# Performance work log

Measured on AMD Instinct MI355X. Metric: run time of the kernel, lower is better.

Reference implementation:

```python
import jax, jax.numpy as jnp
import numpy as np

T, B, I = 1024, 32, 1024   # seq_len, batch, input_size
H = 1024                   # hidden_size
NH = 8                     # n_heads
HS = H // NH               # head_size = 128


def setup_inputs() -> dict:
    key = jax.random.key(0)
    kx, kih, khh, kb = jax.random.split(key, 4)
    lim = (1.0 / HS) ** 0.5
    xs = jax.random.normal(kx, (T, B, I), dtype=jnp.float32)
    weight_ih = jax.random.uniform(kih, (NH, 4 * HS, I), minval=-lim, maxval=lim, dtype=jnp.float32)
    weight_hh = jax.random.uniform(khh, (NH, 4 * HS, HS), minval=-lim, maxval=lim, dtype=jnp.float32)
    bias = jax.random.uniform(kb, (NH, 4 * HS), minval=-lim, maxval=lim, dtype=jnp.float32)
    return {"xs": xs, "weight_ih": weight_ih, "weight_hh": weight_hh, "bias": bias}


def reference(xs, weight_ih, weight_hh, bias):
    # xs: [T, B, I]; weight_ih: [NH, 4*HS, I]; weight_hh: [NH, 4*HS, HS]; bias: [NH, 4*HS]
    t, b, _ = xs.shape
    nh, k4, hs = weight_hh.shape
    zeros = jnp.zeros((b, nh, hs), dtype=xs.dtype)

    def step(state, x):
        h, c, m, n = state  # each [B, NH, HS]
        lin = (jnp.einsum('hki,bi->bhk', weight_ih, x)
               + jnp.einsum('hkd,bhd->bhk', weight_hh, h)
               + bias)  # [B, NH, 4*HS]
        i, f, z, o = jnp.split(lin, 4, axis=2)
        z = jnp.tanh(z)
        o = jax.nn.sigmoid(o)
        m_new = jnp.maximum(f + m, i)          # stabilizer state
        i_e = jnp.exp(i - m_new)
        f_e = jnp.exp(f + m - m_new)
        c_new = f_e * c + i_e * z
        n_new = f_e * n + i_e
        h_new = o * (c_new / n_new)
        return (h_new, c_new, m_new, n_new), h_new.reshape(b, nh * hs)

    _, hs_out = jax.lax.scan(step, (zeros, zeros, zeros, zeros), xs)
    return hs_out  # [T, B, H]
```

## Files before the change

### kernel.cpp

```cpp
#include <hip/hip_runtime.h>
#include <stdint.h>
#include <stddef.h>

#define TT   1024
#define BB   32
#define II   1024
#define HH   1024
#define NHH  8
#define HSS  128
#define N4   4096

typedef _Float16 h8 __attribute__((ext_vector_type(8)));
typedef _Float16 h4 __attribute__((ext_vector_type(4)));
typedef float    f4 __attribute__((ext_vector_type(4)));

#define GLDS16(G, L) __builtin_amdgcn_global_load_lds(                      \
    (__attribute__((address_space(1))) void*)(G),                           \
    (__attribute__((address_space(3))) void*)(L), 16, 0, 0)

__global__ void prep_kernel(const float* __restrict__ whh, float* __restrict__ whhT,
                            float* __restrict__ st, float* __restrict__ hst) {
  int idx = blockIdx.x * blockDim.x + threadIdx.x;
  int stride = gridDim.x * blockDim.x;
  for (int i = idx; i < NHH * 512 * HSS; i += stride) {
    int head = i >> 16;
    int rem = i & 65535;
    int n = rem >> 7, k = rem & 127;
    whhT[(size_t)(head * HSS + k) * 512 + n] = whh[i];
  }
  for (int i = idx; i < 3 * BB * NHH * HSS; i += stride) st[i] = 0.0f;
  for (int i = idx; i < BB * NHH * HSS; i += stride) hst[i] = 0.0f;
}

__global__ __launch_bounds__(256) void convert_split(
    const float* __restrict__ src, _Float16* __restrict__ hi,
    _Float16* __restrict__ lo, int n4) {
  int idx = blockIdx.x * blockDim.x + threadIdx.x;
  int stride = gridDim.x * blockDim.x;
  for (int i = idx; i < n4; i += stride) {
    const float4 x = *(const float4*)&src[(size_t)i * 4];
    _Float16 h0 = (_Float16)x.x, h1 = (_Float16)x.y,
             h2 = (_Float16)x.z, h3 = (_Float16)x.w;
    _Float16 l0 = (_Float16)((x.x - (float)h0) * 2048.0f);
    _Float16 l1 = (_Float16)((x.y - (float)h1) * 2048.0f);
    _Float16 l2 = (_Float16)((x.z - (float)h2) * 2048.0f);
    _Float16 l3 = (_Float16)((x.w - (float)h3) * 2048.0f);
    h4 hv = {h0, h1, h2, h3};
    h4 lv = {l0, l1, l2, l3};
    *(h4*)&hi[(size_t)i * 4] = hv;
    *(h4*)&lo[(size_t)i * 4] = lv;
  }
}

__global__ __launch_bounds__(256, 2) void gemm_gates_mfma(
    const _Float16* __restrict__ Ah, const _Float16* __restrict__ Al,
    const _Float16* __restrict__ Bh, const _Float16* __restrict__ Bl,
    const float* __restrict__ bias, float* __restrict__ C) {
  __shared__ __align__(16) _Float16 sAh[128 * 32];
  __shared__ __align__(16) _Float16 sAl[128 * 32];
  __shared__ __align__(16) _Float16 sBh[128 * 32];
  __shared__ __align__(16) _Float16 sBl[128 * 32];

  const int tid = threadIdx.x;
  const int lane = tid & 63;
  const int wave = tid >> 6;
  const long r0 = (long)blockIdx.y * 128;
  const long c0 = (long)blockIdx.x * 128;
  const int wr = (wave >> 1) * 64;
  const int wc = (wave & 1) * 64;

  f4 acc1[4][4], acc2[4][4];
#pragma unroll
  for (int i = 0; i < 4; ++i)
#pragma unroll
    for (int j = 0; j < 4; ++j) { acc1[i][j] = (f4)0.0f; acc2[i][j] = (f4)0.0f; }

  const int sRow = tid >> 2;
  const int sKh = (tid & 3) * 8;
  const _Float16* gAh = Ah + (r0 + sRow) * 1024 + sKh;
  const _Float16* gAl = Al + (r0 + sRow) * 1024 + sKh;
  const _Float16* gBh = Bh + (c0 + sRow) * 1024 + sKh;
  const _Float16* gBl = Bl + (c0 + sRow) * 1024 + sKh;
  _Float16* lAh = &sAh[sRow * 32 + sKh];
  _Float16* lAl = &sAl[sRow * 32 + sKh];
  _Float16* lBh = &sBh[sRow * 32 + sKh];
  _Float16* lBl = &sBl[sRow * 32 + sKh];

  const int fRow = lane & 15;
  const int fK = (lane >> 4) * 8;

  for (int kt = 0; kt < 32; ++kt) {
    const int k0 = kt * 32;
    GLDS16(gAh + k0, lAh);
    GLDS16(gAh + k0 + 64 * 1024, lAh + 64 * 32);
    GLDS16(gAl + k0, lAl);
    GLDS16(gAl + k0 + 64 * 1024, lAl + 64 * 32);
    GLDS16(gBh + k0, lBh);
    GLDS16(gBh + k0 + 64 * 1024, lBh + 64 * 32);
    GLDS16(gBl + k0, lBl);
    GLDS16(gBl + k0 + 64 * 1024, lBl + 64 * 32);
    __syncthreads();

    h8 fBh[4], fBl[4];
#pragma unroll
    for (int j = 0; j < 4; ++j) {
      fBh[j] = *(const h8*)&sBh[(wc + j * 16 + fRow) * 32 + fK];
      fBl[j] = *(const h8*)&sBl[(wc + j * 16 + fRow) * 32 + fK];
    }
#pragma unroll
    for (int i = 0; i < 4; ++i) {
      h8 ah = *(const h8*)&sAh[(wr + i * 16 + fRow) * 32 + fK];
      h8 al = *(const h8*)&sAl[(wr + i * 16 + fRow) * 32 + fK];
#pragma unroll
      for (int j = 0; j < 4; ++j) {
        acc1[i][j] = __builtin_amdgcn_mfma_f32_16x16x32_f16(ah, fBh[j], acc1[i][j], 0, 0, 0);
        acc2[i][j] = __builtin_amdgcn_mfma_f32_16x16x32_f16(ah, fBl[j], acc2[i][j], 0, 0, 0);
        acc2[i][j] = __builtin_amdgcn_mfma_f32_16x16x32_f16(al, fBh[j], acc2[i][j], 0, 0, 0);
      }
    }
    __syncthreads();
  }

  const int rgrp = (lane >> 4) * 4;
#pragma unroll
  for (int j = 0; j < 4; ++j) {
    const long col = c0 + wc + j * 16 + fRow;
    const float bj = bias[col];
#pragma unroll
    for (int i = 0; i < 4; ++i) {
      const long row = r0 + wr + i * 16 + rgrp;
#pragma unroll
      for (int q = 0; q < 4; ++q) {
        C[(row + q) * (long)N4 + col] =
            acc1[i][j][q] + acc2[i][j][q] * (1.0f / 2048.0f) + bj;
      }
    }
  }
}

__device__ __forceinline__ float fast_sigmoid(float x) {
  return 1.0f / (1.0f + __expf(-x));
}
__device__ __forceinline__ float fast_tanh(float x) {
  return 1.0f - 2.0f / (__expf(2.0f * x) + 1.0f);
}

__global__ __launch_bounds__(512, 2) void scan_f32(
    const float* __restrict__ gates, const float* __restrict__ whhT,
    float* __restrict__ out,
    float* __restrict__ stc, float* __restrict__ stn, float* __restrict__ stm,
    float* __restrict__ hst, int t0, int chp) {
  __shared__ float hbuf[128];
  __shared__ float pre[512];
  const int tid = threadIdx.x;
  const int head = blockIdx.x >> 5, b = blockIdx.x & 31;
  const int g = tid >> 7;

  float W[128];
#pragma unroll
  for (int k = 0; k < 128; ++k) W[k] = whhT[(size_t)(head * HSS + k) * 512 + tid];

  float c = 0.f, nn = 0.f, m = 0.f;
  if (tid < 128) {
    int si = (b * NHH + head) * HSS + tid;
    c = stc[si]; nn = stn[si]; m = stm[si];
    hbuf[tid] = hst[si];
  }
  __syncthreads();

  const size_t gbase = (size_t)b * N4 + head * 512 + tid;
  float gcur = gates[gbase];

  for (int t = 0; t < chp; ++t) {
    float gnext = 0.0f;
    if (t + 1 < chp) gnext = gates[gbase + (size_t)(t + 1) * 32 * N4];

    float a0 = 0.f, a1 = 0.f;
#pragma unroll
    for (int k4 = 0; k4 < 16; ++k4) {
      float4 h0 = *(const float4*)&hbuf[k4 * 4];
      float4 h1 = *(const float4*)&hbuf[64 + k4 * 4];
      a0 = fmaf(W[k4 * 4 + 0], h0.x, a0); a0 = fmaf(W[k4 * 4 + 1], h0.y, a0);
      a0 = fmaf(W[k4 * 4 + 2], h0.z, a0); a0 = fmaf(W[k4 * 4 + 3], h0.w, a0);
      a1 = fmaf(W[64 + k4 * 4 + 0], h1.x, a1); a1 = fmaf(W[64 + k4 * 4 + 1], h1.y, a1);
      a1 = fmaf(W[64 + k4 * 4 + 2], h1.z, a1); a1 = fmaf(W[64 + k4 * 4 + 3], h1.w, a1);
    }
    float pv = gcur + (a0 + a1);
    if (g == 2) pv = fast_tanh(pv);
    else if (g == 3) pv = fast_sigmoid(pv);
    pre[tid] = pv;
    __syncthreads();

    if (tid < 128) {
      float iv = pre[tid], fv = pre[128 + tid];
      float zt = pre[256 + tid], og = pre[384 + tid];
      float a = fv + m;
      float mn = fmaxf(a, iv);
      float fe = __expf(a - mn);
      float ie = __expf(iv - mn);
      c = fe * c + ie * zt;
      nn = fe * nn + ie;
      m = mn;
      float h = og * (c / nn);
      out[(size_t)(t0 + t) * (BB * HH) + (size_t)b * HH + head * HSS + tid] = h;
      hbuf[tid] = h;
    }
    __syncthreads();
    gcur = gnext;
  }

  if (tid < 128) {
    int si = (b * NHH + head) * HSS + tid;
    stc[si] = c; stn[si] = nn; stm[si] = m;
    hst[si] = hbuf[tid];
  }
}

extern "C" void kernel_launch(void* const* d_in, const int* in_sizes, int n_in,
                              void* d_out, int out_size, void* d_ws, size_t ws_size,
                              hipStream_t stream) {
  const float* xs   = (const float*)d_in[0];
  const float* wih  = (const float*)d_in[1];
  const float* whh  = (const float*)d_in[2];
  const float* bias = (const float*)d_in[3];
  float* out = (float*)d_out;
  char* ws = (char*)d_ws;

  float* whhT = (float*)(ws + 0);
  float* stc  = (float*)(ws + 2097152);
  float* stn  = (float*)(ws + 2228224);
  float* stm  = (float*)(ws + 2359296);
  float* hst  = (float*)(ws + 2490368);
  _Float16* Bh = (_Float16*)(ws + 2621440);
  _Float16* Bl = (_Float16*)(ws + 11010048);
  const size_t base = 19398656;

  int ch = 256;
  while (ch > 8 && base + (size_t)ch * 655360 > ws_size) ch >>= 1;
  _Float16* Ahp = (_Float16*)(ws + base);
  _Float16* Alp = (_Float16*)(ws + base + (size_t)ch * 65536);
  float* gts = (float*)(ws + base + (size_t)ch * 131072);
  const int nch = TT / ch;

  prep_kernel<<<256, 256, 0, stream>>>(whh, whhT, stc, hst);
  convert_split<<<1024, 256, 0, stream>>>(wih, Bh, Bl, N4 * II / 4);

  for (int cix = 0; cix < nch; ++cix) {
    convert_split<<<1024, 256, 0, stream>>>(xs + (size_t)cix * ch * BB * II,
                                            Ahp, Alp, ch * BB * II / 4);
    dim3 g(32, (unsigned)(ch * 32 / 128));
    gemm_gates_mfma<<<g, 256, 0, stream>>>(Ahp, Alp, Bh, Bl, bias, gts);
    scan_f32<<<256, 512, 0, stream>>>(gts, whhT, out, stc, stn, stm, hst,
                                      cix * ch, ch);
  }
}
```

Measured before the change: 2.285 ms.

## Compute recurrent matvec with split-fp16 MFMA and double-buffered hidden state

Replaces the per-thread fp32 FMA recurrent matvec in the scan kernel with 16x16x32 fp16 MFMA instructions, using a hi/lo fp16 split of both weight_hh and h to keep near-fp32 accuracy. Each wave computes 16 hidden columns for all four gates, so the pointwise xLSTM update runs directly in the owner lanes. This removes the gate-exchange shared buffer and one barrier per step, and double-buffers h in LDS. Only one of the 16 MFMA rows is useful (batch is per-block), so most MFMA work is wasted, and the split loses a little precision.

```diff
diff --git a/kernel.cpp b/kernel.cpp
--- a/kernel.cpp
+++ b/kernel.cpp
@@ -18,16 +18,9 @@
     (__attribute__((address_space(1))) void*)(G),                           \
     (__attribute__((address_space(3))) void*)(L), 16, 0, 0)
 
-__global__ void prep_kernel(const float* __restrict__ whh, float* __restrict__ whhT,
-                            float* __restrict__ st, float* __restrict__ hst) {
+__global__ void prep_kernel(float* __restrict__ st, float* __restrict__ hst) {
   int idx = blockIdx.x * blockDim.x + threadIdx.x;
   int stride = gridDim.x * blockDim.x;
-  for (int i = idx; i < NHH * 512 * HSS; i += stride) {
-    int head = i >> 16;
-    int rem = i & 65535;
-    int n = rem >> 7, k = rem & 127;
-    whhT[(size_t)(head * HSS + k) * 512 + n] = whh[i];
-  }
   for (int i = idx; i < 3 * BB * NHH * HSS; i += stride) st[i] = 0.0f;
   for (int i = idx; i < BB * NHH * HSS; i += stride) hst[i] = 0.0f;
 }
@@ -145,74 +138,116 @@
   return 1.0f - 2.0f / (__expf(2.0f * x) + 1.0f);
 }
 
-__global__ __launch_bounds__(512, 2) void scan_f32(
-    const float* __restrict__ gates, const float* __restrict__ whhT,
-    float* __restrict__ out,
+__global__ __launch_bounds__(512, 2) void scan_mfma(
+    const float* __restrict__ gates, const _Float16* __restrict__ whh_hi,
+    const _Float16* __restrict__ whh_lo, float* __restrict__ out,
     float* __restrict__ stc, float* __restrict__ stn, float* __restrict__ stm,
     float* __restrict__ hst, int t0, int chp) {
-  __shared__ float hbuf[128];
-  __shared__ float pre[512];
+  __shared__ __align__(16) _Float16 hbuf[2][2][128];
   const int tid = threadIdx.x;
+  const int lane = tid & 63;
+  const int w = tid >> 6;
   const int head = blockIdx.x >> 5, b = blockIdx.x & 31;
-  const int g = tid >> 7;
-
-  float W[128];
-#pragma unroll
-  for (int k = 0; k < 128; ++k) W[k] = whhT[(size_t)(head * HSS + k) * 512 + tid];
-
-  float c = 0.f, nn = 0.f, m = 0.f;
-  if (tid < 128) {
-    int si = (b * NHH + head) * HSS + tid;
+  const int fcol = lane & 15;
+  const int fk = (lane >> 4) * 8;
+  const int d = w * 16 + fcol;
+  const bool owner = (lane < 16);
+
+  h8 Bh[4][4], Bl[4][4];
+#pragma unroll
+  for (int g = 0; g < 4; ++g)
+#pragma unroll
+    for (int kt = 0; kt < 4; ++kt) {
+      const size_t off = ((size_t)((head * 4 + g) * 128 + d)) * 128 + kt * 32 + fk;
+      Bh[g][kt] = *(const h8*)&whh_hi[off];
+      Bl[g][kt] = *(const h8*)&whh_lo[off];
+    }
+
+  float c = 0.f, nn = 0.f, m = 0.f, hlast = 0.f;
+  const int si = (b * NHH + head) * HSS + d;
+  if (owner) {
     c = stc[si]; nn = stn[si]; m = stm[si];
-    hbuf[tid] = hst[si];
+    float h0 = hst[si];
+    hlast = h0;
+    _Float16 hh = (_Float16)h0;
+    _Float16 hl = (_Float16)((h0 - (float)hh) * 2048.0f);
+    hbuf[0][0][d] = hh;
+    hbuf[0][1][d] = hl;
   }
   __syncthreads();
 
-  const size_t gbase = (size_t)b * N4 + head * 512 + tid;
-  float gcur = gates[gbase];
-
+  const float* gptr = gates + (size_t)b * N4 + head * 512 + d;
+  float gc[4] = {0.f, 0.f, 0.f, 0.f};
+  if (owner) {
+#pragma unroll
+    for (int g = 0; g < 4; ++g) gc[g] = gptr[g * 128];
+  }
+
+  int cur = 0;
   for (int t = 0; t < chp; ++t) {
-    float gnext = 0.0f;
-    if (t + 1 < chp) gnext = gates[gbase + (size_t)(t + 1) * 32 * N4];
-
-    float a0 = 0.f, a1 = 0.f;
-#pragma unroll
-    for (int k4 = 0; k4 < 16; ++k4) {
-      float4 h0 = *(const float4*)&hbuf[k4 * 4];
-      float4 h1 = *(const float4*)&hbuf[64 + k4 * 4];
-      a0 = fmaf(W[k4 * 4 + 0], h0.x, a0); a0 = fmaf(W[k4 * 4 + 1], h0.y, a0);
-      a0 = fmaf(W[k4 * 4 + 2], h0.z, a0); a0 = fmaf(W[k4 * 4 + 3], h0.w, a0);
-      a1 = fmaf(W[64 + k4 * 4 + 0], h1.x, a1); a1 = fmaf(W[64 + k4 * 4 + 1], h1.y, a1);
-      a1 = fmaf(W[64 + k4 * 4 + 2], h1.z, a1); a1 = fmaf(W[64 + k4 * 4 + 3], h1.w, a1);
-    }
-    float pv = gcur + (a0 + a1);
-    if (g == 2) pv = fast_tanh(pv);
-    else if (g == 3) pv = fast_sigmoid(pv);
-    pre[tid] = pv;
-    __syncthreads();
-
-    if (tid < 128) {
-      float iv = pre[tid], fv = pre[128 + tid];
-      float zt = pre[256 + tid], og = pre[384 + tid];
-      float a = fv + m;
-      float mn = fmaxf(a, iv);
+    h8 Ah[4], Al[4];
+#pragma unroll
+    for (int kt = 0; kt < 4; ++kt) {
+      Ah[kt] = *(const h8*)&hbuf[cur][0][kt * 32 + fk];
+      Al[kt] = *(const h8*)&hbuf[cur][1][kt * 32 + fk];
+    }
+
+    float gn[4] = {0.f, 0.f, 0.f, 0.f};
+    if (owner && t + 1 < chp) {
+      const float* gp = gptr + (size_t)(t + 1) * 32 * N4;
+#pragma unroll
+      for (int g = 0; g < 4; ++g) gn[g] = gp[g * 128];
+    }
+
+    f4 c1[4], c2[4];
+#pragma unroll
+    for (int g = 0; g < 4; ++g) {
+      f4 z = (f4)0.0f;
+      z[0] = owner ? gc[g] : 0.0f;
+      c1[g] = z;
+      c2[g] = (f4)0.0f;
+    }
+#pragma unroll
+    for (int kt = 0; kt < 4; ++kt)
+#pragma unroll
+      for (int g = 0; g < 4; ++g) {
+        c1[g] = __builtin_amdgcn_mfma_f32_16x16x32_f16(Ah[kt], Bh[g][kt], c1[g], 0, 0, 0);
+        c2[g] = __builtin_amdgcn_mfma_f32_16x16x32_f16(Ah[kt], Bl[g][kt], c2[g], 0, 0, 0);
+        c2[g] = __builtin_amdgcn_mfma_f32_16x16x32_f16(Al[kt], Bh[g][kt], c2[g], 0, 0, 0);
+      }
+
+    if (owner) {
+      const float k = 1.0f / 2048.0f;
+      float pi = c1[0][0] + c2[0][0] * k;
+      float pf = c1[1][0] + c2[1][0] * k;
+      float pz = c1[2][0] + c2[2][0] * k;
+      float po = c1[3][0] + c2[3][0] * k;
+      float a = pf + m;
+      float mn = fmaxf(a, pi);
       float fe = __expf(a - mn);
-      float ie = __expf(iv - mn);
+      float ie = __expf(pi - mn);
+      float zt = fast_tanh(pz);
+      float og = fast_sigmoid(po);
       c = fe * c + ie * zt;
       nn = fe * nn + ie;
       m = mn;
       float h = og * (c / nn);
-      out[(size_t)(t0 + t) * (BB * HH) + (size_t)b * HH + head * HSS + tid] = h;
-      hbuf[tid] = h;
+      hlast = h;
+      out[(size_t)(t0 + t) * (BB * HH) + (size_t)b * HH + head * HSS + d] = h;
+      _Float16 hh = (_Float16)h;
+      _Float16 hl = (_Float16)((h - (float)hh) * 2048.0f);
+      hbuf[cur ^ 1][0][d] = hh;
+      hbuf[cur ^ 1][1][d] = hl;
     }
     __syncthreads();
-    gcur = gnext;
-  }
-
-  if (tid < 128) {
-    int si = (b * NHH + head) * HSS + tid;
+    cur ^= 1;
+#pragma unroll
+    for (int g = 0; g < 4; ++g) gc[g] = gn[g];
+  }
+
+  if (owner) {
     stc[si] = c; stn[si] = nn; stm[si] = m;
-    hst[si] = hbuf[tid];
+    hst[si] = hlast;
   }
 }
 
@@ -226,13 +261,14 @@
   float* out = (float*)d_out;
   char* ws = (char*)d_ws;
 
-  float* whhT = (float*)(ws + 0);
-  float* stc  = (float*)(ws + 2097152);
-  float* stn  = (float*)(ws + 2228224);
-  float* stm  = (float*)(ws + 2359296);
-  float* hst  = (float*)(ws + 2490368);
-  _Float16* Bh = (_Float16*)(ws + 2621440);
-  _Float16* Bl = (_Float16*)(ws + 11010048);
+  float* stc = (float*)(ws + 0);
+  float* stn = (float*)(ws + 131072);
+  float* stm = (float*)(ws + 262144);
+  float* hst = (float*)(ws + 393216);
+  _Float16* Whi = (_Float16*)(ws + 524288);
+  _Float16* Wlo = (_Float16*)(ws + 1572864);
+  _Float16* Bh  = (_Float16*)(ws + 2621440);
+  _Float16* Bl  = (_Float16*)(ws + 11010048);
   const size_t base = 19398656;
 
   int ch = 256;
@@ -242,7 +278,8 @@
   float* gts = (float*)(ws + base + (size_t)ch * 131072);
   const int nch = TT / ch;
 
-  prep_kernel<<<256, 256, 0, stream>>>(whh, whhT, stc, hst);
+  prep_kernel<<<256, 256, 0, stream>>>(stc, hst);
+  convert_split<<<1024, 256, 0, stream>>>(whh, Whi, Wlo, NHH * 512 * HSS / 4);
   convert_split<<<1024, 256, 0, stream>>>(wih, Bh, Bl, N4 * II / 4);
 
   for (int cix = 0; cix < nch; ++cix) {
@@ -250,7 +287,7 @@
                                             Ahp, Alp, ch * BB * II / 4);
     dim3 g(32, (unsigned)(ch * 32 / 128));
     gemm_gates_mfma<<<g, 256, 0, stream>>>(Ahp, Alp, Bh, Bl, bias, gts);
-    scan_f32<<<256, 512, 0, stream>>>(gts, whhT, out, stc, stn, stm, hst,
-                                      cix * ch, ch);
-  }
-}
+    scan_mfma<<<256, 512, 0, stream>>>(gts, Whi, Wlo, out, stc, stn, stm, hst,
+                                       cix * ch, ch);
+  }
+}
```

Result: no change. 2.304 ms (+0.9%).
